# Kernel tuning notes

Hardware: AMD Instinct MI355X
Metric: run time of the kernel (lower is better)

The kernel has to match this reference:

```python
import jax, jax.numpy as jnp
import numpy as np
import math

B, NRES, RPR = 1, 384, 3
L = NRES * RPR          # 1152 rigids
CS, CZ = 256, 128
CH, H, PQ, PV = 16, 8, 8, 12


def _ln(x, scale, bias):
    mu = jnp.mean(x, axis=-1, keepdims=True)
    var = jnp.var(x, axis=-1, keepdims=True)
    return (x - mu) * jax.lax.rsqrt(var + 1e-5) * scale + bias


def _quat_to_rot(q):
    q = q / jnp.linalg.norm(q, axis=-1, keepdims=True)
    w, x, y, z = q[..., 0], q[..., 1], q[..., 2], q[..., 3]
    r = jnp.stack([
        1 - 2 * (y * y + z * z), 2 * (x * y - w * z), 2 * (x * z + w * y),
        2 * (x * y + w * z), 1 - 2 * (x * x + z * z), 2 * (y * z - w * x),
        2 * (x * z - w * y), 2 * (y * z + w * x), 1 - 2 * (x * x + y * y),
    ], axis=-1)
    return r.reshape(q.shape[:-1] + (3, 3))


def setup_inputs() -> dict:
    key = jax.random.key(0)
    ks = jax.random.split(key, 20)
    s = jax.random.normal(ks[0], (B, L, CS), jnp.float32)
    z = jax.random.normal(ks[1], (B, NRES, NRES, CZ), jnp.float32)
    rot = _quat_to_rot(jax.random.normal(ks[2], (B, L, 4), jnp.float32))
    trans = 10.0 * jax.random.normal(ks[3], (B, L, 3), jnp.float32)
    mask = jnp.ones((B, L), jnp.float32)
    rigid_to_res_idx = jnp.broadcast_to(jnp.arange(L, dtype=jnp.int32) // RPR, (B, L))
    w = lambda k, sh: 0.02 * jax.random.normal(k, sh, jnp.float32)
    return {
        "s": s, "z": z, "rot": rot, "trans": trans, "mask": mask,
        "ln_s_scale": jnp.ones((CS,), jnp.float32), "ln_s_bias": jnp.zeros((CS,), jnp.float32),
        "ln_z_scale": jnp.ones((CZ,), jnp.float32), "ln_z_bias": jnp.zeros((CZ,), jnp.float32),
        "w_q": w(ks[4], (CS, H * CH)), "w_k": w(ks[5], (CS, H * CH)), "w_v": w(ks[6], (CS, H * CH)),
        "w_qp": w(ks[7], (CS, H * PQ * 3)), "w_kp": w(ks[8], (CS, H * PQ * 3)), "w_vp": w(ks[9], (CS, H * PV * 3)),
        "w_b": w(ks[10], (CZ, H)),
        "head_weights": jnp.full((H,), 0.5413, jnp.float32),  # softplus^-1(1)
        "w_out": w(ks[11], (H * (CH + CZ + PV * 4), CS)),
        "b_out": jnp.zeros((CS,), jnp.float32),
        "rigid_to_res_idx": rigid_to_res_idx,
    }


def reference(s, z, rot, trans, mask, ln_s_scale, ln_s_bias, ln_z_scale, ln_z_bias,
              w_q, w_k, w_v, w_qp, w_kp, w_vp, w_b, head_weights, w_out, b_out,
              rigid_to_res_idx):
    b_, l_ = s.shape[0], s.shape[1]
    idx = rigid_to_res_idx[0]                       # [L] rigid -> residue, shared over batch
    s_ln = _ln(s, ln_s_scale, ln_s_bias)            # [B,L,CS]
    z_ln = _ln(z, ln_z_scale, ln_z_bias)            # [B,N,N,CZ]

    q = (s_ln @ w_q).reshape(b_, l_, H, CH)
    k = (s_ln @ w_k).reshape(b_, l_, H, CH)
    v = (s_ln @ w_v).reshape(b_, l_, H, CH)

    # local points, then rigid-transform to global frame: x_g = R x + t
    q_p = (s_ln @ w_qp).reshape(b_, l_, H, PQ, 3)
    k_p = (s_ln @ w_kp).reshape(b_, l_, H, PQ, 3)
    v_p = (s_ln @ w_vp).reshape(b_, l_, H, PV, 3)
    t5 = trans[:, :, None, None, :]
    q_g = jnp.einsum("blij,blhpj->blhpi", rot, q_p) + t5
    k_g = jnp.einsum("blij,blhpj->blhpi", rot, k_p) + t5
    v_g = jnp.einsum("blij,blhpj->blhpi", rot, v_p) + t5

    # scalar qk term
    a = jnp.einsum("blhc,bjhc->bhlj", q, k) * math.sqrt(1.0 / (3 * CH))
    # pair bias, broadcast residue-pair -> rigid-pair
    b_res = z_ln @ w_b                                # [B,N,N,H]
    b_full = b_res[:, idx][:, :, idx]                 # [B,L,L,H]
    a = a + math.sqrt(1.0 / 3) * jnp.transpose(b_full, (0, 3, 1, 2))
    # point-distance term: ||q-k||^2 = |q|^2 + |k|^2 - 2 q.k (summed over P,3)
    hw = jax.nn.softplus(head_weights) * math.sqrt(1.0 / (3 * (PQ * 9.0 / 2)))
    qq = jnp.sum(q_g * q_g, axis=(-1, -2)).transpose(0, 2, 1)   # [B,H,L]
    kk = jnp.sum(k_g * k_g, axis=(-1, -2)).transpose(0, 2, 1)
    qk = jnp.einsum("blhpc,bjhpc->bhlj", q_g, k_g)
    d2 = qq[:, :, :, None] + kk[:, :, None, :] - 2.0 * qk
    a = a - 0.5 * d2 * hw[None, :, None, None]
    a = a + (mask[:, None, None, :] - 1.0) * 1e9
    attn = jax.nn.softmax(a, axis=-1)                 # [B,H,L,L]

    o = jnp.einsum("bhlj,bjhc->blhc", attn, v)        # [B,L,H,CH]
    o_pt_g = jnp.einsum("bhlj,bjhpc->blhpc", attn, v_g)
    # back to local frame of query rigid: R^T (x - t)
    o_pt = jnp.einsum("blji,blhpj->blhpi", rot, o_pt_g - t5)
    o_pt_norm = jnp.sqrt(jnp.sum(o_pt * o_pt, axis=-1) + 1e-8)  # [B,L,H,PV]
    # pair output: sum attention over rigids belonging to each key residue
    attn_res = attn.reshape(b_, H, l_, NRES, RPR).sum(-1)       # [B,H,L,N]
    z_l = z_ln[:, idx]                                           # [B,L,N,CZ]
    o_pair = jnp.einsum("bhln,blnc->blhc", attn_res, z_l)        # [B,L,H,CZ]

    cat = jnp.concatenate(
        [o, o_pt.reshape(b_, l_, H, PV * 3), o_pt_norm, o_pair], axis=-1
    ).reshape(b_, l_, H * (CH + PV * 4 + CZ))
    return cat @ w_out + b_out                        # [B,L,CS]
```

## Files before the change

### kernel.cpp

```cpp
#include <hip/hip_runtime.h>
#include <hip/hip_bf16.h>

#define L 1152
#define NRES 384
#define CS 256
#define CZ 128
#define H 8
#define CH 16
#define PQ 8
#define PV 12
#define PSTR 1088

#define OFF_SLN  0L
#define OFF_PROJ 294912L
#define OFF_WPK  1548288L
#define OFF_QCAT 1826816L
#define OFF_KCAT 2232320L
#define OFF_VCAT 2637824L
#define OFF_BRES 3227648L
#define OFF_MURS 4407296L
#define OFF_ATTN 4702208L
#define OFF_CAT  15319040L
#define OFF_PAV  18286592L
#define OFF_POP  21825536L
#define OFF_ARES 26544128L
#define OFF_PCAT 30083072L

__global__ __launch_bounds__(256) void k_pre(
    const float* wq, const float* wk, const float* wv,
    const float* wqp, const float* wkp, const float* wvp, float* wpack,
    const float* s, const float* lnss, const float* lnsb, float* sln,
    const float* z, const float* lnzs, const float* lnzb,
    const float* wb, float* murs, float* bres_t){
  int bx = blockIdx.x, t = threadIdx.x;
  if(bx < 256){
    int k = bx;
    for(int c=t; c<PSTR; c+=256){
      float v;
      if(c<128)        v = wq [(long)k*128 + c];
      else if(c<256)   v = wk [(long)k*128 + c-128];
      else if(c<384)   v = wv [(long)k*128 + c-256];
      else if(c<576)   v = wqp[(long)k*192 + c-384];
      else if(c<768)   v = wkp[(long)k*192 + c-576];
      else if(c<1056)  v = wvp[(long)k*288 + c-768];
      else             v = 0.f;
      wpack[(long)k*PSTR + c] = v;
    }
    return;
  }
  if(bx < 256 + L){
    int l = bx - 256;
    __shared__ float red[CS];
    float x = s[(long)l*CS + t];
    red[t] = x; __syncthreads();
    for(int st=128; st>0; st>>=1){ if(t<st) red[t]+=red[t+st]; __syncthreads(); }
    float mu = red[0] * (1.f/CS); __syncthreads();
    float d = x - mu;
    red[t] = d*d; __syncthreads();
    for(int st=128; st>0; st>>=1){ if(t<st) red[t]+=red[t+st]; __syncthreads(); }
    float var = red[0]*(1.f/CS);
    sln[(long)l*CS + t] = d*rsqrtf(var + 1e-5f)*lnss[t] + lnsb[t];
    return;
  }
  {
    long rp0 = (long)(bx - 256 - L)*32;
    int r = t>>3, part = t&7;
    long rp = rp0 + r;
    __shared__ __align__(16) float swb[8*132];
    __shared__ float SB[8][2];
    const float4* z4 = (const float4*)z;
    float4 x0 = z4[rp*32 + part*4 + 0];
    float4 x1 = z4[rp*32 + part*4 + 1];
    float4 x2 = z4[rp*32 + part*4 + 2];
    float4 x3 = z4[rp*32 + part*4 + 3];
    #pragma unroll
    for(int k2=0;k2<4;k2++){
      int e = t + k2*256; int h = e>>7, c = e&127;
      swb[h*132 + c] = lnzs[c]*wb[(long)c*8 + h];
    }
    __syncthreads();
    if(t < 64){
      int h = t>>3, seg = t&7;
      float S=0, Bv=0;
      #pragma unroll
      for(int i=0;i<16;i++){
        int c = seg*16+i;
        S  += swb[h*132+c];
        Bv += lnzb[c]*wb[(long)c*8 + h];
      }
      #pragma unroll
      for(int off=1;off<8;off<<=1){ S += __shfl_xor(S,off,64); Bv += __shfl_xor(Bv,off,64); }
      if(seg==0){ SB[h][0]=S; SB[h][1]=Bv; }
    }
    float s1 = x0.x+x0.y+x0.z+x0.w + x1.x+x1.y+x1.z+x1.w
             + x2.x+x2.y+x2.z+x2.w + x3.x+x3.y+x3.z+x3.w;
    float s2 = x0.x*x0.x+x0.y*x0.y+x0.z*x0.z+x0.w*x0.w
             + x1.x*x1.x+x1.y*x1.y+x1.z*x1.z+x1.w*x1.w
             + x2.x*x2.x+x2.y*x2.y+x2.z*x2.z+x2.w*x2.w
             + x3.x*x3.x+x3.y*x3.y+x3.z*x3.z+x3.w*x3.w;
    #pragma unroll
    for(int off=1;off<8;off<<=1){ s1 += __shfl_xor(s1,off,64); s2 += __shfl_xor(s2,off,64); }
    float mu = s1*(1.f/CZ);
    float var = s2*(1.f/CZ) - mu*mu;
    float rstd = rsqrtf(var + 1e-5f);
    if(part==0){ murs[rp*2]=mu; murs[rp*2+1]=rstd; }
    float acc[8];
    const float4* swb4 = (const float4*)swb;
    #pragma unroll
    for(int h=0;h<8;h++){
      float4 wa = swb4[h*33 + part*4 + 0];
      float4 wbv= swb4[h*33 + part*4 + 1];
      float4 wc = swb4[h*33 + part*4 + 2];
      float4 wd = swb4[h*33 + part*4 + 3];
      acc[h] = x0.x*wa.x + x0.y*wa.y + x0.z*wa.z + x0.w*wa.w
             + x1.x*wbv.x+ x1.y*wbv.y+ x1.z*wbv.z+ x1.w*wbv.w
             + x2.x*wc.x + x2.y*wc.y + x2.z*wc.z + x2.w*wc.w
             + x3.x*wd.x + x3.y*wd.y + x3.z*wd.z + x3.w*wd.w;
    }
    #pragma unroll
    for(int off=1;off<8;off<<=1){
      #pragma unroll
      for(int h=0;h<8;h++) acc[h] += __shfl_xor(acc[h],off,64);
    }
    __syncthreads();
    if(part==0){
      #pragma unroll
      for(int h=0;h<8;h++)
        bres_t[(long)h*147456 + rp] = rstd*(acc[h] - mu*SB[h][0]) + SB[h][1];
    }
  }
}

__global__ __launch_bounds__(256) void k_proj(const float* sln, const float* wpack, float* proj){
  int l0 = blockIdx.x*64, c0 = blockIdx.y*64, t = threadIdx.x;
  __shared__ float a_s[32][68];
  __shared__ __align__(16) float w_s[32][68];
  int tr = t>>4, tc = t&15;
  float4 acc[4] = {{0,0,0,0},{0,0,0,0},{0,0,0,0},{0,0,0,0}};
  for(int kc=0; kc<8; kc++){
    int k0 = kc*32;
    {
      int row = t>>2, kk0 = (t&3)*8;
      const float4* src = (const float4*)(sln + (long)(l0+row)*256 + k0 + kk0);
      float4 v0 = src[0], v1 = src[1];
      a_s[kk0+0][row]=v0.x; a_s[kk0+1][row]=v0.y; a_s[kk0+2][row]=v0.z; a_s[kk0+3][row]=v0.w;
      a_s[kk0+4][row]=v1.x; a_s[kk0+5][row]=v1.y; a_s[kk0+6][row]=v1.z; a_s[kk0+7][row]=v1.w;
    }
    #pragma unroll
    for(int kk2=0; kk2<2; kk2++){
      int kk = (t>>4) + 16*kk2;
      *(float4*)&w_s[kk][(t&15)*4] = *(const float4*)(wpack + (long)(k0+kk)*PSTR + c0 + (t&15)*4);
    }
    __syncthreads();
    #pragma unroll 8
    for(int kk=0; kk<32; kk++){
      float4 a4 = *(const float4*)&a_s[kk][tr*4];
      float4 b4 = *(const float4*)&w_s[kk][tc*4];
      acc[0].x+=a4.x*b4.x; acc[0].y+=a4.x*b4.y; acc[0].z+=a4.x*b4.z; acc[0].w+=a4.x*b4.w;
      acc[1].x+=a4.y*b4.x; acc[1].y+=a4.y*b4.y; acc[1].z+=a4.y*b4.z; acc[1].w+=a4.y*b4.w;
      acc[2].x+=a4.z*b4.x; acc[2].y+=a4.z*b4.y; acc[2].z+=a4.z*b4.z; acc[2].w+=a4.z*b4.w;
      acc[3].x+=a4.w*b4.x; acc[3].y+=a4.w*b4.y; acc[3].z+=a4.w*b4.z; acc[3].w+=a4.w*b4.w;
    }
    __syncthreads();
  }
  #pragma unroll
  for(int r=0;r<4;r++)
    *(float4*)(proj + (long)(l0 + tr*4 + r)*PSTR + c0 + tc*4) = acc[r];
}

__global__ __launch_bounds__(256) void k_rigid(const float* proj, const float* rot, const float* trans,
                        const float* mask, const float* hws,
                        float* qcat, float* kcat, float* vcat){
  int l = blockIdx.x, t = threadIdx.x;
  __shared__ float R[9], T[3], hwS[8], qgs[192], kgs[192];
  if(t<9) R[t]=rot[(long)l*9+t];
  if(t<3) T[t]=trans[(long)l*3+t];
  if(t>=16 && t<24) hwS[t-16] = log1pf(expf(hws[t-16]))*0.09622504486493764f;
  __syncthreads();
  const float* pr = proj + (long)l*PSTR;
  if(t<128){
    int h=t>>4, c=t&15;
    qcat[((long)h*44 + c)*L + l] = 0.14433756729740643f * pr[t];
    kcat[((long)h*44 + c)*L + l] = pr[128+t];
    vcat[((long)h*L + l)*64 + c] = pr[256+t];
  }
  if(t < 192){
    int h=t/24, m=t%24, p=m/3, i=m%3;
    float qa = R[i*3+0]*pr[384+h*24+p*3+0] + R[i*3+1]*pr[384+h*24+p*3+1]
             + R[i*3+2]*pr[384+h*24+p*3+2] + T[i];
    float ka = R[i*3+0]*pr[576+h*24+p*3+0] + R[i*3+1]*pr[576+h*24+p*3+1]
             + R[i*3+2]*pr[576+h*24+p*3+2] + T[i];
    qgs[t]=qa; kgs[t]=ka;
    qcat[((long)h*44 + 16 + m)*L + l] = hwS[h]*qa;
    kcat[((long)h*44 + 16 + m)*L + l] = ka;
  }
  for(int it=t; it<288; it+=256){
    int h=it/36, m=it%36, p=m/3, i=m%3;
    float a = R[i*3+0]*pr[768+h*36+p*3+0] + R[i*3+1]*pr[768+h*36+p*3+1]
            + R[i*3+2]*pr[768+h*36+p*3+2] + T[i];
    vcat[((long)h*L + l)*64 + 16 + m] = a;
  }
  if(t < 96){
    int h=t/12, d=t%12;
    vcat[((long)h*L + l)*64 + 52 + d] = 0.f;
  }
  __syncthreads();
  if(t < 8){
    float qq=0, kk=0;
    #pragma unroll
    for(int m=0;m<24;m++){ qq += qgs[t*24+m]*qgs[t*24+m]; kk += kgs[t*24+m]*kgs[t*24+m]; }
    qcat[((long)t*44 + 40)*L + l] = -0.5f*hwS[t]*qq;
    kcat[((long)t*44 + 40)*L + l] = -0.5f*hwS[t]*kk + (mask[l]-1.f)*1e9f;
  }
}

__global__ __launch_bounds__(256) void k_scores(const float* qcat, const float* kcat,
                         const float* bres_t, float* attn){
  int l0 = blockIdx.x*32, j0 = blockIdx.y*128, h = blockIdx.z;
  int t = threadIdx.x;
  __shared__ __align__(16) float q_t[44*36];
  __shared__ __align__(16) float k_t[44*132];
  __shared__ float bp[12*44];
  int rl0 = l0/3, rj0 = j0/3;
  {
    const float* srcq = qcat + (long)h*44*L + l0;
    for(int i=t; i<44*32; i+=256){
      int c = i>>5, ll = i&31;
      q_t[c*36 + ll] = srcq[(long)c*L + ll];
    }
    const float* srck = kcat + (long)h*44*L + j0;
    for(int i=t; i<44*128; i+=256){
      int c = i>>7, jj = i&127;
      k_t[c*132 + jj] = srck[(long)c*L + jj];
    }
    const float* bb = bres_t + (long)h*147456;
    for(int i=t; i<12*44; i+=256){
      int r = i/44, c = i-r*44;
      int rr = rl0+r, cc = rj0+c;
      bp[i] = (rr<NRES && cc<NRES) ? bb[(long)rr*NRES + cc] : 0.f;
    }
  }
  __syncthreads();
  int lg = t>>5, jg = t&31;
  float acc[4][4] = {};
  #pragma unroll 4
  for(int c=0;c<40;c++){
    float4 qv = *(const float4*)&q_t[c*36 + lg*4];
    float4 kv = *(const float4*)&k_t[c*132 + jg*4];
    acc[0][0]+=qv.x*kv.x; acc[0][1]+=qv.x*kv.y; acc[0][2]+=qv.x*kv.z; acc[0][3]+=qv.x*kv.w;
    acc[1][0]+=qv.y*kv.x; acc[1][1]+=qv.y*kv.y; acc[1][2]+=qv.y*kv.z; acc[1][3]+=qv.y*kv.w;
    acc[2][0]+=qv.z*kv.x; acc[2][1]+=qv.z*kv.y; acc[2][2]+=qv.z*kv.z; acc[2][3]+=qv.z*kv.w;
    acc[3][0]+=qv.w*kv.x; acc[3][1]+=qv.w*kv.y; acc[3][2]+=qv.w*kv.z; acc[3][3]+=qv.w*kv.w;
  }
  float4 colc = *(const float4*)&k_t[40*132 + jg*4];
  int jb = j0 + jg*4;
  int rj0i = (jb  )/3 - rj0;
  int rj1i = (jb+1)/3 - rj0;
  int rj2i = (jb+2)/3 - rj0;
  int rj3i = (jb+3)/3 - rj0;
  #pragma unroll
  for(int r=0;r<4;r++){
    int row = lg*4+r;
    float rowc = q_t[40*36 + row];
    const float* bpr = &bp[((l0+row)/3 - rl0)*44];
    float4 o;
    o.x = acc[r][0] + rowc + colc.x + 0.5773502691896258f*bpr[rj0i];
    o.y = acc[r][1] + rowc + colc.y + 0.5773502691896258f*bpr[rj1i];
    o.z = acc[r][2] + rowc + colc.z + 0.5773502691896258f*bpr[rj2i];
    o.w = acc[r][3] + rowc + colc.w + 0.5773502691896258f*bpr[rj3i];
    *(float4*)(attn + ((long)h*L + l0+row)*L + jb) = o;
  }
}

__global__ __launch_bounds__(256) void k_rowstat(float* attn, float* ares){
  long row = (long)blockIdx.x*4 + (threadIdx.x>>6);
  int lane = threadIdx.x & 63;
  int w = threadIdx.x >> 6;
  __shared__ float es[4][1152];
  float* p = attn + row*L;
  float v[18];
  float m=-1e30f;
  #pragma unroll
  for(int i=0;i<18;i++){ v[i]=p[lane + i*64]; m=fmaxf(m,v[i]); }
  #pragma unroll
  for(int off=1;off<64;off<<=1) m=fmaxf(m,__shfl_xor(m,off,64));
  float s=0;
  #pragma unroll
  for(int i=0;i<18;i++){ v[i]=__expf(v[i]-m); s+=v[i]; }
  #pragma unroll
  for(int off=1;off<64;off<<=1) s+=__shfl_xor(s,off,64);
  float inv = 1.f/s;
  #pragma unroll
  for(int i=0;i<18;i++){
    float pv = v[i]*inv;
    p[lane + i*64] = pv;
    es[w][lane + i*64] = pv;
  }
  __syncthreads();
  #pragma unroll
  for(int q=0;q<6;q++){
    int n = lane + q*64;
    ares[row*NRES + n] = es[w][3*n] + es[w][3*n+1] + es[w][3*n+2];
  }
}

__global__ __launch_bounds__(256) void k_av(const float* attn, const float* vcat, float* pav){
  int lb = blockIdx.x, h = blockIdx.y, sp = blockIdx.z, t = threadIdx.x;
  int l0 = lb*64;
  __shared__ __align__(16) float a_s[64][68];
  __shared__ __align__(16) float v_s[64][68];
  int lgrp = t>>4, dgrp = t&15;
  float4 acc[4] = {{0,0,0,0},{0,0,0,0},{0,0,0,0},{0,0,0,0}};
  const float* abase = attn + ((long)h*L + l0)*L;
  int al = t>>2, jj0s = (t&3)*16;
  for(int jc=sp*3; jc<sp*3+3; jc++){
    int j0 = jc*64;
    {
      const float4* src = (const float4*)(abase + (long)al*L + j0 + jj0s);
      float4 p0 = src[0], p1 = src[1], p2 = src[2], p3 = src[3];
      a_s[jj0s+ 0][al]=p0.x; a_s[jj0s+ 1][al]=p0.y; a_s[jj0s+ 2][al]=p0.z; a_s[jj0s+ 3][al]=p0.w;
      a_s[jj0s+ 4][al]=p1.x; a_s[jj0s+ 5][al]=p1.y; a_s[jj0s+ 6][al]=p1.z; a_s[jj0s+ 7][al]=p1.w;
      a_s[jj0s+ 8][al]=p2.x; a_s[jj0s+ 9][al]=p2.y; a_s[jj0s+10][al]=p2.z; a_s[jj0s+11][al]=p2.w;
      a_s[jj0s+12][al]=p3.x; a_s[jj0s+13][al]=p3.y; a_s[jj0s+14][al]=p3.z; a_s[jj0s+15][al]=p3.w;
    }
    {
      int jj = t>>2, seg = t&3;
      const float4* src = (const float4*)(vcat + ((long)h*L + j0 + jj)*64 + seg*16);
      float4 q0=src[0], q1=src[1], q2=src[2], q3=src[3];
      float4* dst = (float4*)&v_s[jj][seg*16];
      dst[0]=q0; dst[1]=q1; dst[2]=q2; dst[3]=q3;
    }
    __syncthreads();
    #pragma unroll 8
    for(int jj=0; jj<64; jj++){
      float4 av = *(const float4*)&a_s[jj][lgrp*4];
      float4 vv = *(const float4*)&v_s[jj][dgrp*4];
      acc[0].x+=av.x*vv.x; acc[0].y+=av.x*vv.y; acc[0].z+=av.x*vv.z; acc[0].w+=av.x*vv.w;
      acc[1].x+=av.y*vv.x; acc[1].y+=av.y*vv.y; acc[1].z+=av.y*vv.z; acc[1].w+=av.y*vv.w;
      acc[2].x+=av.z*vv.x; acc[2].y+=av.z*vv.y; acc[2].z+=av.z*vv.z; acc[2].w+=av.z*vv.w;
      acc[3].x+=av.w*vv.x; acc[3].y+=av.w*vv.y; acc[3].z+=av.w*vv.z; acc[3].w+=av.w*vv.w;
    }
    __syncthreads();
  }
  #pragma unroll
  for(int r=0;r<4;r++)
    *(float4*)(pav + (((long)sp*H + h)*L + l0 + lgrp*4 + r)*64 + dgrp*4) = acc[r];
}

#define OPAIR_STEP(Z0,Z1,Z2,Z3,NB) { \
    float4 a0 = *(const float4*)&ar[0][th][NB]; \
    float4 a1 = *(const float4*)&ar[1][th][NB]; \
    float4 a2 = *(const float4*)&ar[2][th][NB]; \
    acc[0][0] += a0.x*Z0.x + a0.y*Z1.x + a0.z*Z2.x + a0.w*Z3.x; \
    acc[0][1] += a0.x*Z0.y + a0.y*Z1.y + a0.z*Z2.y + a0.w*Z3.y; \
    acc[0][2] += a0.x*Z0.z + a0.y*Z1.z + a0.z*Z2.z + a0.w*Z3.z; \
    acc[0][3] += a0.x*Z0.w + a0.y*Z1.w + a0.z*Z2.w + a0.w*Z3.w; \
    acc[1][0] += a1.x*Z0.x + a1.y*Z1.x + a1.z*Z2.x + a1.w*Z3.x; \
    acc[1][1] += a1.x*Z0.y + a1.y*Z1.y + a1.z*Z2.y + a1.w*Z3.y; \
    acc[1][2] += a1.x*Z0.z + a1.y*Z1.z + a1.z*Z2.z + a1.w*Z3.z; \
    acc[1][3] += a1.x*Z0.w + a1.y*Z1.w + a1.z*Z2.w + a1.w*Z3.w; \
    acc[2][0] += a2.x*Z0.x + a2.y*Z1.x + a2.z*Z2.x + a2.w*Z3.x; \
    acc[2][1] += a2.x*Z0.y + a2.y*Z1.y + a2.z*Z2.y + a2.w*Z3.y; \
    acc[2][2] += a2.x*Z0.z + a2.y*Z1.z + a2.z*Z2.z + a2.w*Z3.z; \
    acc[2][3] += a2.x*Z0.w + a2.y*Z1.w + a2.z*Z2.w + a2.w*Z3.w; }

__global__ __launch_bounds__(256) void k_opair(const float* ares, const float* z, const float* murs,
                        const float* sc, const int* ridx, float* po){
  int r=blockIdx.x, sp=blockIdx.y, t=threadIdx.x;
  __shared__ __align__(16) float ar[3][H][96];
  __shared__ __align__(16) float mrs[96*2];
  __shared__ float S1s[24];
  int rl = ridx[r*3];
  int n0 = sp*96;
  int tc = t&31, th = t>>5;
  const float* zbase = z + ((long)(rl*NRES + n0))*CZ + tc*4;
  float4 zc0 = *(const float4*)(zbase + 0L*CZ);
  float4 zc1 = *(const float4*)(zbase + 1L*CZ);
  float4 zc2 = *(const float4*)(zbase + 2L*CZ);
  float4 zc3 = *(const float4*)(zbase + 3L*CZ);
  for(int i=t;i<192;i+=256) mrs[i]=murs[((long)rl*NRES + n0)*2 + i];
  __syncthreads();
  for(int it=t; it<3*H*96; it+=256){
    int lo = it/(H*96);
    int rem = it - lo*(H*96);
    int h = rem/96, n = rem - h*96;
    ar[lo][h][n] = ares[((long)h*L + r*3+lo)*NRES + n0 + n] * mrs[n*2+1];
  }
  __syncthreads();
  if(t<192){
    int row=t>>3, seg=t&7;
    const float* arr = ((const float*)ar) + row*96 + seg*12;
    const float* mur = mrs + seg*24;
    float s1=0;
    #pragma unroll
    for(int q2=0;q2<12;q2++) s1 += arr[q2]*mur[q2*2];
    s1 += __shfl_xor(s1,1,64); s1 += __shfl_xor(s1,2,64); s1 += __shfl_xor(s1,4,64);
    if(seg==0) S1s[row]=s1;
  }
  __syncthreads();
  float acc[3][4]={};
  for(int nb=0; nb<88; nb+=8){
    float4 zn0 = *(const float4*)(zbase + (long)(nb+4)*CZ);
    float4 zn1 = *(const float4*)(zbase + (long)(nb+5)*CZ);
    float4 zn2 = *(const float4*)(zbase + (long)(nb+6)*CZ);
    float4 zn3 = *(const float4*)(zbase + (long)(nb+7)*CZ);
    OPAIR_STEP(zc0,zc1,zc2,zc3, nb);
    zc0 = *(const float4*)(zbase + (long)(nb+ 8)*CZ);
    zc1 = *(const float4*)(zbase + (long)(nb+ 9)*CZ);
    zc2 = *(const float4*)(zbase + (long)(nb+10)*CZ);
    zc3 = *(const float4*)(zbase + (long)(nb+11)*CZ);
    OPAIR_STEP(zn0,zn1,zn2,zn3, nb+4);
  }
  {
    float4 zn0 = *(const float4*)(zbase + 92L*CZ);
    float4 zn1 = *(const float4*)(zbase + 93L*CZ);
    float4 zn2 = *(const float4*)(zbase + 94L*CZ);
    float4 zn3 = *(const float4*)(zbase + 95L*CZ);
    OPAIR_STEP(zc0,zc1,zc2,zc3, 88);
    OPAIR_STEP(zn0,zn1,zn2,zn3, 92);
  }
  float4 sc4 = *(const float4*)(sc + tc*4);
  #pragma unroll
  for(int lo=0;lo<3;lo++){
    float s1v = S1s[lo*8+th];
    float4 o = { sc4.x*(acc[lo][0]-s1v), sc4.y*(acc[lo][1]-s1v),
                 sc4.z*(acc[lo][2]-s1v), sc4.w*(acc[lo][3]-s1v) };
    *(float4*)(po + ((long)sp*L + (long)(r*3+lo))*1024 + th*128 + tc*4) = o;
  }
}

__global__ __launch_bounds__(256) void k_post(const float* pav, const float* rot, const float* trans,
                        const float* po, const float* bi, float* cat){
  int bx = blockIdx.x, t = threadIdx.x;
  if(bx < 288){
    int lb = bx % 36, h = bx / 36;
    int l0 = lb*32;
    __shared__ __align__(16) float fin_s[32][64];
    #pragma unroll
    for(int k=0;k<2;k++){
      int fi = t + k*256;
      int l = fi>>4, c4 = fi&15;
      long base = (((long)h)*L + l0 + l)*64 + c4*4;
      float4 r = {0,0,0,0};
      #pragma unroll
      for(int p=0;p<6;p++){
        float4 a = *(const float4*)(pav + (long)p*589824 + base);
        r.x+=a.x; r.y+=a.y; r.z+=a.z; r.w+=a.w;
      }
      *(float4*)&fin_s[l][c4*4] = r;
    }
    __syncthreads();
    for(int it=t; it<32*16; it+=256){
      int l=it>>4, c=it&15;
      cat[(long)(l0+l)*1536 + h*192 + c] = fin_s[l][c];
    }
    for(int it=t; it<32*12; it+=256){
      int l=it/12, p=it%12;
      long gl = l0+l;
      float og0 = fin_s[l][16+p*3+0]-trans[gl*3+0];
      float og1 = fin_s[l][16+p*3+1]-trans[gl*3+1];
      float og2 = fin_s[l][16+p*3+2]-trans[gl*3+2];
      float* crow = cat + gl*1536 + h*192;
      float nrm=0;
      #pragma unroll
      for(int i=0;i<3;i++){
        float v = rot[gl*9+0+i]*og0 + rot[gl*9+3+i]*og1 + rot[gl*9+6+i]*og2;
        crow[16+p*3+i]=v; nrm+=v*v;
      }
      crow[52+p]=sqrtf(nrm+1e-8f);
    }
    return;
  }
  {
    int i = (bx-288)*256 + t;
    const float4* p = (const float4*)po;
    float4 a = p[i], b = p[i + 294912], c = p[i + 589824], d = p[i + 884736];
    int l = i>>8, rem = i&255;
    int h = rem>>5, c4 = rem&31;
    float4 bv = ((const float4*)bi)[c4];
    float4 r = {a.x+b.x+c.x+d.x+bv.x, a.y+b.y+c.y+d.y+bv.y,
                a.z+b.z+c.z+d.z+bv.z, a.w+b.w+c.w+d.w+bv.w};
    ((float4*)cat)[(long)l*384 + h*48 + 16 + c4] = r;
  }
}

__global__ __launch_bounds__(256) void k_final(const float* cat, const float* wout, float* pcat){
  int l0 = blockIdx.x*64, c0 = blockIdx.y*64, kp = blockIdx.z, t = threadIdx.x;
  __shared__ __align__(16) float a_s[64][68];
  __shared__ __align__(16) float w_s[64][68];
  int lgrp = t>>4, cgrp = t&15;
  float4 acc[4] = {{0,0,0,0},{0,0,0,0},{0,0,0,0},{0,0,0,0}};
  int al = t>>2, ks0 = (t&3)*16;
  for(int kc=0; kc<3; kc++){
    int k0 = kp*192 + kc*64;
    {
      const float4* src = (const float4*)(cat + (long)(l0+al)*1536 + k0 + ks0);
      float4 p0 = src[0], p1 = src[1], p2 = src[2], p3 = src[3];
      a_s[ks0+ 0][al]=p0.x; a_s[ks0+ 1][al]=p0.y; a_s[ks0+ 2][al]=p0.z; a_s[ks0+ 3][al]=p0.w;
      a_s[ks0+ 4][al]=p1.x; a_s[ks0+ 5][al]=p1.y; a_s[ks0+ 6][al]=p1.z; a_s[ks0+ 7][al]=p1.w;
      a_s[ks0+ 8][al]=p2.x; a_s[ks0+ 9][al]=p2.y; a_s[ks0+10][al]=p2.z; a_s[ks0+11][al]=p2.w;
      a_s[ks0+12][al]=p3.x; a_s[ks0+13][al]=p3.y; a_s[ks0+14][al]=p3.z; a_s[ks0+15][al]=p3.w;
    }
    {
      int kk = t>>2, seg = t&3;
      const float4* src = (const float4*)(wout + (long)(k0+kk)*256 + c0 + seg*16);
      float4 q0=src[0], q1=src[1], q2=src[2], q3=src[3];
      float4* dst = (float4*)&w_s[kk][seg*16];
      dst[0]=q0; dst[1]=q1; dst[2]=q2; dst[3]=q3;
    }
    __syncthreads();
    #pragma unroll 8
    for(int kk=0; kk<64; kk++){
      float4 av = *(const float4*)&a_s[kk][lgrp*4];
      float4 wv = *(const float4*)&w_s[kk][cgrp*4];
      acc[0].x+=av.x*wv.x; acc[0].y+=av.x*wv.y; acc[0].z+=av.x*wv.z; acc[0].w+=av.x*wv.w;
      acc[1].x+=av.y*wv.x; acc[1].y+=av.y*wv.y; acc[1].z+=av.y*wv.z; acc[1].w+=av.y*wv.w;
      acc[2].x+=av.z*wv.x; acc[2].y+=av.z*wv.y; acc[2].z+=av.z*wv.z; acc[2].w+=av.z*wv.w;
      acc[3].x+=av.w*wv.x; acc[3].y+=av.w*wv.y; acc[3].z+=av.w*wv.z; acc[3].w+=av.w*wv.w;
    }
    __syncthreads();
  }
  #pragma unroll
  for(int r=0;r<4;r++)
    *(float4*)(pcat + ((long)kp*L + l0 + lgrp*4 + r)*256 + c0 + cgrp*4) = acc[r];
}

__global__ __launch_bounds__(256) void k_redout(const float* pcat, const float* bout, float* out){
  int i = blockIdx.x*256 + threadIdx.x;
  const float4* p = (const float4*)pcat;
  float4 bv = ((const float4*)bout)[i&63];
  float4 r = bv;
  #pragma unroll
  for(int p8=0;p8<8;p8++){
    float4 a = p[i + (long)p8*73728];
    r.x+=a.x; r.y+=a.y; r.z+=a.z; r.w+=a.w;
  }
  ((float4*)out)[i] = r;
}

extern "C" void kernel_launch(void* const* d_in, const int* in_sizes, int n_in,
                              void* d_out, int out_size, void* d_ws, size_t ws_size,
                              hipStream_t stream) {
  const float* s      = (const float*)d_in[0];
  const float* z      = (const float*)d_in[1];
  const float* rot    = (const float*)d_in[2];
  const float* trans  = (const float*)d_in[3];
  const float* mask   = (const float*)d_in[4];
  const float* lnss   = (const float*)d_in[5];
  const float* lnsb   = (const float*)d_in[6];
  const float* lnzs   = (const float*)d_in[7];
  const float* lnzb   = (const float*)d_in[8];
  const float* wq     = (const float*)d_in[9];
  const float* wk     = (const float*)d_in[10];
  const float* wv     = (const float*)d_in[11];
  const float* wqp    = (const float*)d_in[12];
  const float* wkp    = (const float*)d_in[13];
  const float* wvp    = (const float*)d_in[14];
  const float* wb     = (const float*)d_in[15];
  const float* hws    = (const float*)d_in[16];
  const float* wout   = (const float*)d_in[17];
  const float* bout   = (const float*)d_in[18];
  const int*  ridx    = (const int*)d_in[19];

  float* ws  = (float*)d_ws;
  float* out = (float*)d_out;

  float* sln  = ws + OFF_SLN;
  float* proj = ws + OFF_PROJ;
  float* wpk  = ws + OFF_WPK;
  float* qcat = ws + OFF_QCAT;
  float* kcat = ws + OFF_KCAT;
  float* vcat = ws + OFF_VCAT;
  float* bres = ws + OFF_BRES;
  float* murs = ws + OFF_MURS;
  float* attn = ws + OFF_ATTN;
  float* cat  = ws + OFF_CAT;
  float* pcat = ws + OFF_PCAT;
  float* pav  = ws + OFF_PAV;
  float* po   = ws + OFF_POP;
  float* ares = ws + OFF_ARES;

  k_pre<<<dim3(256 + L + NRES*NRES/32), dim3(256), 0, stream>>>(
      wq, wk, wv, wqp, wkp, wvp, wpk,
      s, lnss, lnsb, sln,
      z, lnzs, lnzb, wb, murs, bres);
  k_proj<<<dim3(18,17), dim3(256), 0, stream>>>(sln, wpk, proj);
  k_rigid<<<dim3(L), dim3(256), 0, stream>>>(proj, rot, trans, mask, hws, qcat, kcat, vcat);
  k_scores<<<dim3(L/32, L/128, H), dim3(256), 0, stream>>>(qcat, kcat, bres, attn);
  k_rowstat<<<dim3(H*L/4), dim3(256), 0, stream>>>(attn, ares);
  k_av<<<dim3(L/64, H, 6), dim3(256), 0, stream>>>(attn, vcat, pav);
  k_opair<<<dim3(NRES, 4), dim3(256), 0, stream>>>(ares, z, murs, lnzs, ridx, po);
  k_post<<<dim3(288 + 1152), dim3(256), 0, stream>>>(pav, rot, trans, po, lnzb, cat);
  k_final<<<dim3(L/64, 4, 8), dim3(256), 0, stream>>>(cat, wout, pcat);
  k_redout<<<dim3(288), dim3(256), 0, stream>>>(pcat, bout, out);
}
```

Before: 305.6 us.

## Fuse exp into score kernel and defer softmax normalization to AV

The score kernel now writes exp(score) directly, so the row-stat kernel only sums each row and stores the reciprocal, without a max pass or writing the normalized matrix back. The AV kernel applies the per-row reciprocal while staging attention tiles. This removes one full read-modify-write of the H×L×L attention matrix. In exchange there is no max subtraction, so large logits could overflow exp; the point-distance term is negative, which probably keeps values bounded.

New measurement: 298.2 us. -2.4%, faster.

```diff
diff --git a/kernel.cpp b/kernel.cpp
--- a/kernel.cpp
+++ b/kernel.cpp
@@ -25,6 +25,7 @@
 #define OFF_POP  21825536L
 #define OFF_ARES 26544128L
 #define OFF_PCAT 30083072L
+#define OFF_RST  32442368L
 
 __global__ __launch_bounds__(256) void k_pre(
     const float* wq, const float* wk, const float* wv,
@@ -264,38 +265,30 @@
     float rowc = q_t[40*36 + row];
     const float* bpr = &bp[((l0+row)/3 - rl0)*44];
     float4 o;
-    o.x = acc[r][0] + rowc + colc.x + 0.5773502691896258f*bpr[rj0i];
-    o.y = acc[r][1] + rowc + colc.y + 0.5773502691896258f*bpr[rj1i];
-    o.z = acc[r][2] + rowc + colc.z + 0.5773502691896258f*bpr[rj2i];
-    o.w = acc[r][3] + rowc + colc.w + 0.5773502691896258f*bpr[rj3i];
+    o.x = __expf(acc[r][0] + rowc + colc.x + 0.5773502691896258f*bpr[rj0i]);
+    o.y = __expf(acc[r][1] + rowc + colc.y + 0.5773502691896258f*bpr[rj1i]);
+    o.z = __expf(acc[r][2] + rowc + colc.z + 0.5773502691896258f*bpr[rj2i]);
+    o.w = __expf(acc[r][3] + rowc + colc.w + 0.5773502691896258f*bpr[rj3i]);
     *(float4*)(attn + ((long)h*L + l0+row)*L + jb) = o;
   }
 }
 
-__global__ __launch_bounds__(256) void k_rowstat(float* attn, float* ares){
+__global__ __launch_bounds__(256) void k_rowstat(const float* attn, float* rstat, float* ares){
   long row = (long)blockIdx.x*4 + (threadIdx.x>>6);
   int lane = threadIdx.x & 63;
   int w = threadIdx.x >> 6;
   __shared__ float es[4][1152];
-  float* p = attn + row*L;
+  const float* p = attn + row*L;
   float v[18];
-  float m=-1e30f;
-  #pragma unroll
-  for(int i=0;i<18;i++){ v[i]=p[lane + i*64]; m=fmaxf(m,v[i]); }
-  #pragma unroll
-  for(int off=1;off<64;off<<=1) m=fmaxf(m,__shfl_xor(m,off,64));
   float s=0;
   #pragma unroll
-  for(int i=0;i<18;i++){ v[i]=__expf(v[i]-m); s+=v[i]; }
+  for(int i=0;i<18;i++){ v[i]=p[lane + i*64]; s+=v[i]; }
   #pragma unroll
   for(int off=1;off<64;off<<=1) s+=__shfl_xor(s,off,64);
   float inv = 1.f/s;
-  #pragma unroll
-  for(int i=0;i<18;i++){
-    float pv = v[i]*inv;
-    p[lane + i*64] = pv;
-    es[w][lane + i*64] = pv;
-  }
+  if(lane==0) rstat[row] = inv;
+  #pragma unroll
+  for(int i=0;i<18;i++) es[w][lane + i*64] = v[i]*inv;
   __syncthreads();
   #pragma unroll
   for(int q=0;q<6;q++){
@@ -304,7 +297,8 @@
   }
 }
 
-__global__ __launch_bounds__(256) void k_av(const float* attn, const float* vcat, float* pav){
+__global__ __launch_bounds__(256) void k_av(const float* attn, const float* vcat,
+                     const float* rstat, float* pav){
   int lb = blockIdx.x, h = blockIdx.y, sp = blockIdx.z, t = threadIdx.x;
   int l0 = lb*64;
   __shared__ __align__(16) float a_s[64][68];
@@ -313,15 +307,20 @@
   float4 acc[4] = {{0,0,0,0},{0,0,0,0},{0,0,0,0},{0,0,0,0}};
   const float* abase = attn + ((long)h*L + l0)*L;
   int al = t>>2, jj0s = (t&3)*16;
+  float irow = rstat[(long)h*L + l0 + al];
   for(int jc=sp*3; jc<sp*3+3; jc++){
     int j0 = jc*64;
     {
       const float4* src = (const float4*)(abase + (long)al*L + j0 + jj0s);
       float4 p0 = src[0], p1 = src[1], p2 = src[2], p3 = src[3];
-      a_s[jj0s+ 0][al]=p0.x; a_s[jj0s+ 1][al]=p0.y; a_s[jj0s+ 2][al]=p0.z; a_s[jj0s+ 3][al]=p0.w;
-      a_s[jj0s+ 4][al]=p1.x; a_s[jj0s+ 5][al]=p1.y; a_s[jj0s+ 6][al]=p1.z; a_s[jj0s+ 7][al]=p1.w;
-      a_s[jj0s+ 8][al]=p2.x; a_s[jj0s+ 9][al]=p2.y; a_s[jj0s+10][al]=p2.z; a_s[jj0s+11][al]=p2.w;
-      a_s[jj0s+12][al]=p3.x; a_s[jj0s+13][al]=p3.y; a_s[jj0s+14][al]=p3.z; a_s[jj0s+15][al]=p3.w;
+      a_s[jj0s+ 0][al]=p0.x*irow; a_s[jj0s+ 1][al]=p0.y*irow;
+      a_s[jj0s+ 2][al]=p0.z*irow; a_s[jj0s+ 3][al]=p0.w*irow;
+      a_s[jj0s+ 4][al]=p1.x*irow; a_s[jj0s+ 5][al]=p1.y*irow;
+      a_s[jj0s+ 6][al]=p1.z*irow; a_s[jj0s+ 7][al]=p1.w*irow;
+      a_s[jj0s+ 8][al]=p2.x*irow; a_s[jj0s+ 9][al]=p2.y*irow;
+      a_s[jj0s+10][al]=p2.z*irow; a_s[jj0s+11][al]=p2.w*irow;
+      a_s[jj0s+12][al]=p3.x*irow; a_s[jj0s+13][al]=p3.y*irow;
+      a_s[jj0s+14][al]=p3.z*irow; a_s[jj0s+15][al]=p3.w*irow;
     }
     {
       int jj = t>>2, seg = t&3;
@@ -579,6 +578,7 @@
   float* pav  = ws + OFF_PAV;
   float* po   = ws + OFF_POP;
   float* ares = ws + OFF_ARES;
+  float* rst  = ws + OFF_RST;
 
   k_pre<<<dim3(256 + L + NRES*NRES/32), dim3(256), 0, stream>>>(
       wq, wk, wv, wqp, wkp, wvp, wpk,
@@ -587,8 +587,8 @@
   k_proj<<<dim3(18,17), dim3(256), 0, stream>>>(sln, wpk, proj);
   k_rigid<<<dim3(L), dim3(256), 0, stream>>>(proj, rot, trans, mask, hws, qcat, kcat, vcat);
   k_scores<<<dim3(L/32, L/128, H), dim3(256), 0, stream>>>(qcat, kcat, bres, attn);
-  k_rowstat<<<dim3(H*L/4), dim3(256), 0, stream>>>(attn, ares);
-  k_av<<<dim3(L/64, H, 6), dim3(256), 0, stream>>>(attn, vcat, pav);
+  k_rowstat<<<dim3(H*L/4), dim3(256), 0, stream>>>(attn, rst, ares);
+  k_av<<<dim3(L/64, H, 6), dim3(256), 0, stream>>>(attn, vcat, rst, pav);
   k_opair<<<dim3(NRES, 4), dim3(256), 0, stream>>>(ares, z, murs, lnzs, ridx, po);
   k_post<<<dim3(288 + 1152), dim3(256), 0, stream>>>(pav, rot, trans, po, lnzb, cat);
   k_final<<<dim3(L/64, 4, 8), dim3(256), 0, stream>>>(cat, wout, pcat);
```
